# Optimization experiments

Hardware: AMD Instinct MI355X
Metric: run time of the kernel (lower is better)

## Reference

```python
import jax, jax.numpy as jnp
import numpy as np

N, E, D_IN, H = 4096, 1024, 256, 64
THETA = 0.01
LN_EPS = 1e-5


def _layer_norm(x, w, b):
    m = x.mean(-1, keepdims=True)
    v = ((x - m) ** 2).mean(-1, keepdims=True)
    return (x - m) * jax.lax.rsqrt(v + LN_EPS) * w + b


def setup_inputs() -> dict:
    key = jax.random.key(0)
    ks = jax.random.split(key, 8)
    xav = lambda k, shp: jax.random.normal(k, shp, jnp.float32) * np.float32(np.sqrt(2.0 / (shp[0] + shp[1])))
    return {
        "adj": jax.random.uniform(ks[0], (N, E), jnp.float32),
        "G": jax.random.normal(ks[1], (N, N), jnp.float32) * 0.02,
        "feats": jax.random.normal(ks[2], (N, D_IN), jnp.float32),
        "W_v_w": xav(ks[3], (H, D_IN)),
        "lin_w": xav(ks[4], (H, D_IN)),
        "w_o_w": xav(ks[5], (1, H)),
        "w_o_b": jnp.zeros((1,), jnp.float32),
        "ln1_w": jnp.ones((H,), jnp.float32),
        "ln1_b": jnp.zeros((H,), jnp.float32),
        "ln2_w": jnp.ones((H,), jnp.float32),
        "ln2_b": jnp.zeros((H,), jnp.float32),
        "kn": 10,
    }


def reference(adj, G, feats, W_v_w, lin_w, w_o_w, w_o_b, ln1_w, ln1_b, ln2_w, ln2_b, kn):
    # adj: (N, E) incidence; torch code transposes then uses adj.t() again,
    # so e_center = feats.T @ adj / edge_degree  -> (D_IN, E)
    e_center = (feats.T @ adj) / adj.sum(0)[None, :]
    f = feats @ W_v_w.T                                   # (N, H) values
    scores = (f @ f.T) / np.float32(np.sqrt(H))           # (N, N)
    attn = jax.nn.softmax(scores, axis=1)
    s = _layer_norm(e_center.T @ lin_w.T, ln1_w, ln1_b)   # (E, H)
    d = _layer_norm(attn @ f, ln2_w, ln2_b)               # (N, H)
    # hadamard_power: scores[m,n] = sum_k w[k]*(s[m,k]-d[n,k])^2 + b
    # expanded to avoid the (E*N, H) broadcast the torch code materializes
    w = w_o_w[0]                                          # (H,)
    ta = ((s * s) @ w)[:, None] + ((d * d) @ w)[None, :] - 2.0 * ((s * w) @ d.T) + w_o_b[0]
    ta = jnp.exp(-ta / np.float32(2 * 20 ** 2))           # (E, N)
    Hm = ta.T                                             # (N, E) soft incidence
    # Generate_G_from_H with unit edge weights, done via row/col scaling
    DV = Hm.sum(1)
    DE = Hm.sum(0)
    invDE = jnp.where(DE > 0, 1.0 / DE, 0.0)
    invDV = jnp.where(DV > 0, DV ** -0.5, 0.0)
    A = (invDV[:, None] * Hm) * invDE[None, :]            # DV2 @ H @ W @ invDE
    B = Hm * invDV[:, None]                               # (DV2 @ H).T side
    G_new = A @ B.T                                       # (N, N)
    return (1.0 - THETA) * G + THETA * G_new
```

## Files before the change

kernel.cpp:

```cpp
#include <hip/hip_runtime.h>
#include <hip/hip_bf16.h>
#include <math.h>

#define NN 4096
#define NE 1024
#define DIN 256
#define HD 64

typedef __hip_bfloat16 bf16;
__device__ __forceinline__ float b2f(bf16 x){ return __bfloat162float(x); }

typedef __attribute__((ext_vector_type(8))) short s16x8;
typedef __attribute__((ext_vector_type(4))) float f32x4;

__device__ __forceinline__ unsigned short f2b_rne(float x){
  unsigned u; __builtin_memcpy(&u, &x, 4);
  u += 0x7fff + ((u>>16)&1);
  return (unsigned short)(u>>16);
}

#define STAGE128(dstbase, PA, strideA, PB, strideB, k0) do{ \
  _Pragma("unroll") \
  for (int it_ = 0; it_ < 4; ++it_){ \
    int r_  = it_*32 + (t>>3); \
    int ss_ = ((t&7) ^ (r_&7))*8; \
    __builtin_amdgcn_global_load_lds( \
      (const __attribute__((address_space(1))) void*)((PA) + (size_t)r_*(strideA) + (k0) + ss_), \
      (__attribute__((address_space(3))) void*)((dstbase) + it_*4096 + t*16), 16, 0, 0); \
    __builtin_amdgcn_global_load_lds( \
      (const __attribute__((address_space(1))) void*)((PB) + (size_t)r_*(strideB) + (k0) + ss_), \
      (__attribute__((address_space(3))) void*)((dstbase) + 16384 + it_*4096 + t*16), 16, 0, 0); \
  } }while(0)

#define COMPUTE64(base) do{ \
  _Pragma("unroll") \
  for (int kk_ = 0; kk_ < 2; ++kk_){ \
    s16x8 a_[4], b_[4]; \
    _Pragma("unroll") \
    for (int mi_ = 0; mi_ < 4; ++mi_){ \
      int row_ = wr*64 + mi_*16 + (lane & 15); \
      int s_   = kk_*4 + (lane >> 4); \
      a_[mi_] = *(const s16x8*)((base) + row_*128 + ((s_ ^ (row_&7))*16)); \
    } \
    _Pragma("unroll") \
    for (int ni_ = 0; ni_ < 4; ++ni_){ \
      int row_ = wc*64 + ni_*16 + (lane & 15); \
      int s_   = kk_*4 + (lane >> 4); \
      b_[ni_] = *(const s16x8*)((base) + 16384 + row_*128 + ((s_ ^ (row_&7))*16)); \
    } \
    _Pragma("unroll") \
    for (int mi_ = 0; mi_ < 4; ++mi_) \
      _Pragma("unroll") \
      for (int ni_ = 0; ni_ < 4; ++ni_) \
        acc[mi_][ni_] = __builtin_amdgcn_mfma_f32_16x16x32_bf16(a_[mi_], b_[ni_], acc[mi_][ni_], 0, 0, 0); \
  } }while(0)

__global__ void k_t2b(const float* __restrict__ src, unsigned short* __restrict__ dst,
                      float* __restrict__ csum){
  __shared__ float Ls[64][65];
  int R = gridDim.x*64, C = gridDim.y*64;
  int r0 = blockIdx.x*64, c0 = blockIdx.y*64;
  int t = threadIdx.x;
  int lr = t>>2, lc = (t&3)*16;
  #pragma unroll
  for (int s = 0; s < 4; ++s){
    float4 v = *(const float4*)(src + (size_t)(r0+lr)*C + c0 + lc + s*4);
    Ls[lr][lc+s*4+0]=v.x; Ls[lr][lc+s*4+1]=v.y; Ls[lr][lc+s*4+2]=v.z; Ls[lr][lc+s*4+3]=v.w;
  }
  __syncthreads();
  if (csum != nullptr && t < 64){
    float s = 0.f;
    #pragma unroll
    for (int r = 0; r < 64; ++r) s += Ls[r][t];
    atomicAdd(&csum[c0 + t], s);
  }
  int wc = t>>3, wr8 = (t&7)*8;
  #pragma unroll
  for (int p = 0; p < 2; ++p){
    int c = wc + p*32;
    s16x8 o;
    #pragma unroll
    for (int e = 0; e < 8; ++e) o[e] = (short)f2b_rne(Ls[wr8+e][c]);
    *(s16x8*)(dst + (size_t)(c0+c)*R + r0 + wr8) = o;
  }
}

__global__ void __launch_bounds__(256, 2)
k_ect_mfma(const unsigned short* __restrict__ fT, const unsigned short* __restrict__ aT,
           float* __restrict__ ecT){
  __shared__ __align__(16) unsigned char sm[65536];
  const int t = threadIdx.x, lane = t & 63, w = t >> 6;
  const int wr = w >> 1, wc = w & 1;
  const int m0 = blockIdx.x*128, n0 = blockIdx.y*128, kb = blockIdx.z*256;
  const unsigned short* PA = fT + (size_t)m0*NN + kb;
  const unsigned short* PB = aT + (size_t)n0*NN + kb;
  f32x4 acc[4][4] = {};
  STAGE128(sm, PA, NN, PB, NN, 0);
  __syncthreads();
  int cur = 0;
  for (int kt = 0; kt < 4; ++kt){
    if (kt < 3) STAGE128(sm + (cur^1)*32768, PA, NN, PB, NN, (kt+1)*64);
    COMPUTE64(sm + cur*32768);
    __syncthreads();
    cur ^= 1;
  }
  #pragma unroll
  for (int mi = 0; mi < 4; ++mi)
    #pragma unroll
    for (int q = 0; q < 4; ++q){
      int c = m0 + wr*64 + mi*16 + (lane>>4)*4 + q;
      #pragma unroll
      for (int ni = 0; ni < 4; ++ni){
        int e = n0 + wc*64 + ni*16 + (lane & 15);
        atomicAdd(&ecT[(size_t)e*DIN + c], acc[mi][ni][q]);
      }
    }
}

__global__ void k_s(const float* __restrict__ ecT, const float* __restrict__ colsum,
                    const float* __restrict__ lin_w,
                    const float* __restrict__ ln1w, const float* __restrict__ ln1b,
                    const float* __restrict__ wow,
                    unsigned short* __restrict__ swb, float* __restrict__ sq_s){
  int e = blockIdx.x, h = threadIdx.x;
  const float* row = ecT + (size_t)e*DIN;
  const float* lw  = lin_w + (size_t)h*DIN;
  float acc = 0.f;
  for (int c = 0; c < DIN; ++c) acc += row[c]*lw[c];
  acc /= colsum[e];
  float tot = acc;
  for (int m=32;m>=1;m>>=1) tot += __shfl_xor(tot,m);
  float mean = tot*(1.f/64.f);
  float dv = acc - mean;
  float vv = dv*dv;
  for (int m=32;m>=1;m>>=1) vv += __shfl_xor(vv,m);
  float y = dv*(1.f/sqrtf(vv*(1.f/64.f)+1e-5f))*ln1w[h] + ln1b[h];
  float wv = wow[h];
  swb[(size_t)e*HD + h] = f2b_rne(y*wv);
  float q = wv*y*y;
  for (int m=32;m>=1;m>>=1) q += __shfl_xor(q,m);
  if (h==0) sq_s[e] = q;
}

__global__ void k_f_full(const float* __restrict__ feats, const float* __restrict__ Wv,
                         unsigned short* __restrict__ fb, unsigned short* __restrict__ fbT){
  __shared__ float As[64][65];
  __shared__ float Bs[64][65];
  __shared__ unsigned short Fs[64][72];
  int i0 = blockIdx.x*64;
  int tid=threadIdx.x, tx=tid&15, ty=tid>>4;
  float acc[4][4]={};
  for (int c0=0;c0<DIN;c0+=64){
    if (c0) __syncthreads();
    for (int idx=tid; idx<4096; idx+=256){
      int r=idx>>6, c=idx&63;
      As[c][r] = feats[(size_t)(i0+r)*DIN + c0+c];
      Bs[c][r] = Wv   [(size_t)r*DIN      + c0+c];
    }
    __syncthreads();
    for (int k=0;k<64;++k){
      float a[4], b[4];
      #pragma unroll
      for (int i=0;i<4;++i) a[i] = As[k][tx*4+i];
      #pragma unroll
      for (int i=0;i<4;++i) b[i] = Bs[k][ty*4+i];
      #pragma unroll
      for (int mi=0;mi<4;++mi)
        #pragma unroll
        for (int ni=0;ni<4;++ni) acc[mi][ni] += a[mi]*b[ni];
    }
  }
  #pragma unroll
  for (int mi=0;mi<4;++mi)
    #pragma unroll
    for (int ni=0;ni<4;++ni)
      Fs[tx*4+mi][ty*4+ni] = f2b_rne(acc[mi][ni]);
  __syncthreads();
  {
    int r = tid>>2, c0b = (tid&3)*16;
    s16x8 v0, v1;
    #pragma unroll
    for (int e=0;e<8;++e){ v0[e] = (short)Fs[r][c0b+e]; v1[e] = (short)Fs[r][c0b+8+e]; }
    *(s16x8*)(fb + (size_t)(i0+r)*HD + c0b)     = v0;
    *(s16x8*)(fb + (size_t)(i0+r)*HD + c0b + 8) = v1;
  }
  {
    int h = tid>>2, n1 = (tid&3)*16;
    s16x8 w0, w1;
    #pragma unroll
    for (int e=0;e<8;++e){ w0[e] = (short)Fs[n1+e][h]; w1[e] = (short)Fs[n1+8+e][h]; }
    *(s16x8*)(fbT + (size_t)h*NN + i0 + n1)     = w0;
    *(s16x8*)(fbT + (size_t)h*NN + i0 + n1 + 8) = w1;
  }
}

#define STAGE_ATTN(buf, j0s) do{ \
  _Pragma("unroll") \
  for (int p_=0;p_<2;++p_){ \
    int r_  = p_*32 + (t>>3); \
    int cs_ = ((t&7) ^ (r_&7))*8; \
    __builtin_amdgcn_global_load_lds( \
      (const __attribute__((address_space(1))) void*)(fb + (size_t)((j0s)+r_)*HD + cs_), \
      (__attribute__((address_space(3))) void*)(sm + (buf)*16384 + p_*4096 + t*16), 16, 0, 0); \
    __builtin_amdgcn_global_load_lds( \
      (const __attribute__((address_space(1))) void*)(fbT + (size_t)r_*NN + (j0s) + cs_), \
      (__attribute__((address_space(3))) void*)(sm + (buf)*16384 + 8192 + p_*4096 + t*16), 16, 0, 0); \
  } }while(0)

__global__ void __launch_bounds__(256)
k_attn(const unsigned short* __restrict__ fb, const unsigned short* __restrict__ fbT,
       float* __restrict__ dpre, float* __restrict__ rowsum){
  __shared__ __align__(16) unsigned char sm[49152];
  const int t  = threadIdx.x;
  const int l  = t & 63;
  const int w  = t >> 6;
  const int g  = l >> 4;
  const int i0 = blockIdx.x*64;
  const int jb0 = blockIdx.y*256;

  s16x8 aQ[2];
  {
    const unsigned short* src = fb + (size_t)(i0 + w*16 + (l&15))*HD + g*8;
    aQ[0] = *(const s16x8*)(src);
    aQ[1] = *(const s16x8*)(src + 32);
  }

  f32x4 acco[4];
  #pragma unroll
  for (int nh=0;nh<4;++nh)
    #pragma unroll
    for (int q=0;q<4;++q) acco[nh][q] = 0.f;
  float rsum[4] = {0.f,0.f,0.f,0.f};

  float* Pw = (float*)(sm + 32768 + w*4096);

  STAGE_ATTN(0, jb0);
  __syncthreads();
  int cur = 0;
  for (int jt = 0; jt < 4; ++jt){
    if (jt < 3) STAGE_ATTN(cur^1, jb0 + (jt+1)*64);
    const unsigned char* B = sm + cur*16384;

    f32x4 accs[4];
    #pragma unroll
    for (int nj=0;nj<4;++nj)
      #pragma unroll
      for (int q=0;q<4;++q) accs[nj][q] = 0.f;
    #pragma unroll
    for (int kk=0; kk<2; ++kk){
      int s = kk*4 + g;
      #pragma unroll
      for (int nj=0;nj<4;++nj){
        int row = nj*16 + (l&15);
        s16x8 b = *(const s16x8*)(B + row*128 + ((s ^ (row&7))*16));
        accs[nj] = __builtin_amdgcn_mfma_f32_16x16x32_bf16(aQ[kk], b, accs[nj], 0,0,0);
      }
    }

    #pragma unroll
    for (int q=0;q<4;++q){
      int i  = g*4 + q;
      int sw = (i&7)<<2;
      #pragma unroll
      for (int nj=0;nj<4;++nj){
        float p = __expf(accs[nj][q]*0.125f);
        rsum[q] += p;
        Pw[i*64 + ((nj*16 + (l&15)) ^ sw)] = p;
      }
    }

    #pragma unroll
    for (int kk=0; kk<2; ++kk){
      int i  = l & 15;
      int sw = (i&7)<<2;
      int jb = g*8 + kk*32;
      f32x4 va = *(const f32x4*)(Pw + i*64 + ( jb      ^ sw));
      f32x4 vb = *(const f32x4*)(Pw + i*64 + ((jb + 4) ^ sw));
      s16x8 pa;
      #pragma unroll
      for (int e=0;e<4;++e){
        float fa = va[e], fbv = vb[e];
        pa[e]   = (short)f2b_rne(fa);
        pa[4+e] = (short)f2b_rne(fbv);
      }
      int s = kk*4 + g;
      #pragma unroll
      for (int nh=0;nh<4;++nh){
        int row = nh*16 + (l&15);
        s16x8 bT = *(const s16x8*)(B + 8192 + row*128 + ((s ^ (row&7))*16));
        acco[nh] = __builtin_amdgcn_mfma_f32_16x16x32_bf16(pa, bT, acco[nh], 0,0,0);
      }
    }
    __syncthreads();
    cur ^= 1;
  }

  #pragma unroll
  for (int q=0;q<4;++q){
    float v = rsum[q];
    v += __shfl_xor(v,1); v += __shfl_xor(v,2);
    v += __shfl_xor(v,4); v += __shfl_xor(v,8);
    if ((l&15)==0) atomicAdd(&rowsum[i0 + w*16 + g*4 + q], v);
  }
  #pragma unroll
  for (int nh=0;nh<4;++nh)
    #pragma unroll
    for (int q=0;q<4;++q)
      atomicAdd(&dpre[(size_t)(i0 + w*16 + g*4 + q)*HD + nh*16 + (l&15)], acco[nh][q]);
}

__global__ void k_dln(const float* __restrict__ dpre, const float* __restrict__ rowsum,
                      const float* __restrict__ ln2w, const float* __restrict__ ln2b,
                      const float* __restrict__ wow,
                      unsigned short* __restrict__ dmatb, float* __restrict__ sq_d){
  int lane = threadIdx.x & 63;
  int n = blockIdx.x*4 + (threadIdx.x>>6);
  float x = dpre[(size_t)n*HD + lane] / rowsum[n];
  float tot = x;
  for (int m=32;m>=1;m>>=1) tot += __shfl_xor(tot,m);
  float mean = tot*(1.f/64.f);
  float dv = x - mean;
  float vv = dv*dv;
  for (int m=32;m>=1;m>>=1) vv += __shfl_xor(vv,m);
  float y = dv*(1.f/sqrtf(vv*(1.f/64.f)+1e-5f))*ln2w[lane] + ln2b[lane];
  dmatb[(size_t)n*HD + lane] = f2b_rne(y);
  float wv = wow[lane];
  float q = wv*y*y;
  for (int m=32;m>=1;m>>=1) q += __shfl_xor(q,m);
  if (lane==0) sq_d[n] = q;
}

__global__ void __launch_bounds__(256)
k_hm(const unsigned short* __restrict__ dmatb, const unsigned short* __restrict__ swb,
     const float* __restrict__ sq_d, const float* __restrict__ sq_s,
     const float* __restrict__ wob, bf16* __restrict__ Hm,
     float* __restrict__ DE, float* __restrict__ DVacc){
  __shared__ __align__(16) unsigned char sm[8192];
  __shared__ float DEp[64];
  const int t = threadIdx.x, l = t & 63, w = t >> 6, g = l >> 4;
  const int n0 = blockIdx.x*64, e0 = blockIdx.y*64;
  #pragma unroll
  for (int p = 0; p < 2; ++p){
    int r  = p*32 + (t>>3);
    int cs = ((t&7) ^ (r&7))*8;
    __builtin_amdgcn_global_load_lds(
      (const __attribute__((address_space(1))) void*)(swb + (size_t)(e0+r)*HD + cs),
      (__attribute__((address_space(3))) void*)(sm + p*4096 + t*16), 16, 0, 0);
  }
  s16x8 aQ[2];
  {
    const unsigned short* src = dmatb + (size_t)(n0 + w*16 + (l&15))*HD + g*8;
    aQ[0] = *(const s16x8*)(src);
    aQ[1] = *(const s16x8*)(src + 32);
  }
  if (t < 64) DEp[t] = 0.f;
  f32x4 accs[4];
  #pragma unroll
  for (int nj=0;nj<4;++nj)
    #pragma unroll
    for (int q=0;q<4;++q) accs[nj][q] = 0.f;
  __syncthreads();
  #pragma unroll
  for (int kk=0; kk<2; ++kk){
    int s = kk*4 + g;
    #pragma unroll
    for (int nj=0;nj<4;++nj){
      int row = nj*16 + (l&15);
      s16x8 b = *(const s16x8*)(sm + row*128 + ((s ^ (row&7))*16));
      accs[nj] = __builtin_amdgcn_mfma_f32_16x16x32_bf16(aQ[kk], b, accs[nj], 0,0,0);
    }
  }
  float bias = wob[0];
  float sqd[4];
  #pragma unroll
  for (int q=0;q<4;++q) sqd[q] = sq_d[n0 + w*16 + g*4 + q];
  float rowp[4] = {0.f,0.f,0.f,0.f};
  #pragma unroll
  for (int nj=0;nj<4;++nj){
    int e = e0 + nj*16 + (l&15);
    float sqs = sq_s[e];
    float colp = 0.f;
    #pragma unroll
    for (int q=0;q<4;++q){
      float ta = sqs + sqd[q] - 2.f*accs[nj][q] + bias;
      float arg = -ta*(1.f/800.f);
      if (!(arg > -88.f)) arg = -88.f;
      if (arg > 60.f)     arg = 60.f;
      int n = n0 + w*16 + g*4 + q;
      bf16 hv = __float2bfloat16(__expf(arg));
      Hm[(size_t)n*NE + e] = hv;
      float vr = b2f(hv);
      rowp[q] += vr;
      colp    += vr;
    }
    atomicAdd(&DEp[nj*16 + (l&15)], colp);
  }
  #pragma unroll
  for (int q=0;q<4;++q){
    float v = rowp[q];
    v += __shfl_xor(v,1); v += __shfl_xor(v,2);
    v += __shfl_xor(v,4); v += __shfl_xor(v,8);
    if ((l&15)==0) atomicAdd(&DVacc[n0 + w*16 + g*4 + q], v);
  }
  __syncthreads();
  if (t < 64) atomicAdd(&DE[e0 + t], DEp[t]);
}

__global__ void k_scale(bf16* __restrict__ Hm, const float* __restrict__ DE){
  int idx = blockIdx.x*256 + threadIdx.x;
  int row = idx >> 7, c8 = idx & 127;
  size_t base = (size_t)row*NE + c8*8;
  s16x8 v = *(const s16x8*)(Hm + base);
  s16x8 o;
  #pragma unroll
  for (int j = 0; j < 8; ++j){
    float de = DE[c8*8 + j];
    float r  = (de > 0.f) ? rsqrtf(de) : 0.f;
    unsigned int ww = ((unsigned int)(unsigned short)v[j]) << 16;
    float fv; __builtin_memcpy(&fv, &ww, 4);
    fv *= r;
    o[j] = (short)f2b_rne(fv);
  }
  *(s16x8*)(Hm + base) = o;
}

__global__ void __launch_bounds__(256, 2)
k_final(const bf16* __restrict__ A2, const float* __restrict__ DVacc,
        const float* __restrict__ G, float* __restrict__ out){
  __shared__ __align__(16) unsigned char sm[128*132*4];
  const int t    = threadIdx.x;
  const int lane = t & 63;
  const int w    = t >> 6;
  const int wr   = w >> 1, wc = w & 1;

  int bid = blockIdx.x;
  int idx = (bid & 7)*66 + (bid >> 3);
  int bi = (int)(32.5f - sqrtf(32.5f*32.5f - 2.f*(float)idx));
  while ((bi+1)*32 - ((bi+1)*bi)/2 <= idx) ++bi;
  while (bi*32 - (bi*(bi-1))/2 > idx) --bi;
  int bj = bi + (idx - (bi*32 - (bi*(bi-1))/2));
  const int i0 = bi*128, j0 = bj*128;

  const bf16* PA = A2 + (size_t)i0*NE;
  const bf16* PB = A2 + (size_t)j0*NE;

  f32x4 acc[4][4] = {};
  STAGE128(sm, PA, NE, PB, NE, 0);
  __syncthreads();
  int cur = 0;
  for (int kt = 0; kt < 16; ++kt){
    if (kt < 15) STAGE128(sm + (cur^1)*32768, PA, NE, PB, NE, (kt+1)*64);
    COMPUTE64(sm + cur*32768);
    __syncthreads();
    cur ^= 1;
  }

  float dvi[4][4], dvj[4];
  #pragma unroll
  for (int mi = 0; mi < 4; ++mi)
    #pragma unroll
    for (int q = 0; q < 4; ++q){
      float v = DVacc[i0 + wr*64 + mi*16 + (lane>>4)*4 + q];
      dvi[mi][q] = (v > 0.f) ? rsqrtf(v) : 0.f;
    }
  #pragma unroll
  for (int ni = 0; ni < 4; ++ni){
    float v = DVacc[j0 + wc*64 + ni*16 + (lane & 15)];
    dvj[ni] = (v > 0.f) ? rsqrtf(v) : 0.f;
  }

  float (*T)[132] = (float(*)[132])sm;
  #pragma unroll
  for (int mi = 0; mi < 4; ++mi)
    #pragma unroll
    for (int ni = 0; ni < 4; ++ni)
      #pragma unroll
      for (int q = 0; q < 4; ++q)
        T[wr*64 + mi*16 + (lane>>4)*4 + q][wc*64 + ni*16 + (lane & 15)] =
          0.01f*(dvi[mi][q]*dvj[ni]*acc[mi][ni][q]);
  __syncthreads();

  #pragma unroll
  for (int it = 0; it < 16; ++it){
    int idx2 = it*256 + t;
    int il = idx2 >> 5;
    int jc = (idx2 & 31)*4;
    size_t o = (size_t)(i0+il)*NN + j0 + jc;
    float4 gv = *(const float4*)(G + o);
    float4 r;
    r.x = 0.99f*gv.x + T[il][jc+0];
    r.y = 0.99f*gv.y + T[il][jc+1];
    r.z = 0.99f*gv.z + T[il][jc+2];
    r.w = 0.99f*gv.w + T[il][jc+3];
    *(float4*)(out + o) = r;
  }

  if (bi == bj) return;
  __syncthreads();
  #pragma unroll
  for (int mi = 0; mi < 4; ++mi)
    #pragma unroll
    for (int ni = 0; ni < 4; ++ni)
      #pragma unroll
      for (int q = 0; q < 4; ++q)
        T[wc*64 + ni*16 + (lane & 15)][wr*64 + mi*16 + (lane>>4)*4 + q] =
          0.01f*(dvi[mi][q]*dvj[ni]*acc[mi][ni][q]);
  __syncthreads();
  #pragma unroll
  for (int it = 0; it < 16; ++it){
    int idx2 = it*256 + t;
    int jl = idx2 >> 5;
    int ic = (idx2 & 31)*4;
    size_t o = (size_t)(j0+jl)*NN + i0 + ic;
    float4 gv = *(const float4*)(G + o);
    float4 r;
    r.x = 0.99f*gv.x + T[jl][ic+0];
    r.y = 0.99f*gv.y + T[jl][ic+1];
    r.z = 0.99f*gv.z + T[jl][ic+2];
    r.w = 0.99f*gv.w + T[jl][ic+3];
    *(float4*)(out + o) = r;
  }
}

extern "C" void kernel_launch(void* const* d_in, const int* in_sizes, int n_in,
                              void* d_out, int out_size, void* d_ws, size_t ws_size,
                              hipStream_t stream){
  const float* adj  = (const float*)d_in[0];
  const float* G    = (const float*)d_in[1];
  const float* feats= (const float*)d_in[2];
  const float* Wv   = (const float*)d_in[3];
  const float* lin  = (const float*)d_in[4];
  const float* wow  = (const float*)d_in[5];
  const float* wob  = (const float*)d_in[6];
  const float* ln1w = (const float*)d_in[7];
  const float* ln1b = (const float*)d_in[8];
  const float* ln2w = (const float*)d_in[9];
  const float* ln2b = (const float*)d_in[10];
  float* out = (float*)d_out;

  float* w = (float*)d_ws;
  float* colsum = w; w += NE;
  float* DE     = w; w += NE;
  float* sq_s   = w; w += NE;
  float* rowsum = w; w += NN;
  float* sq_d   = w; w += NN;
  float* DVacc  = w; w += NN;
  float* ecT    = w; w += NE*DIN;
  float* dpre   = w; w += NN*HD;
  unsigned short* swb    = (unsigned short*)w; w += NE*HD/2;
  unsigned short* dmatb  = (unsigned short*)w; w += NN*HD/2;
  unsigned short* fbm    = (unsigned short*)w; w += NN*HD/2;
  unsigned short* fbT    = (unsigned short*)w; w += NN*HD/2;
  unsigned short* featsT = (unsigned short*)w; w += NN*DIN/2;
  bf16*  Hm     = (bf16*)w;
  unsigned short* adjT = (unsigned short*)Hm;

  hipMemsetAsync(colsum, 0, NE*sizeof(float), stream);
  hipMemsetAsync(DE,     0, NE*sizeof(float), stream);
  hipMemsetAsync(rowsum, 0, NN*sizeof(float), stream);
  hipMemsetAsync(DVacc,  0, NN*sizeof(float), stream);
  hipMemsetAsync(ecT,    0, (size_t)NE*DIN*sizeof(float), stream);
  hipMemsetAsync(dpre,   0, (size_t)NN*HD*sizeof(float), stream);

  k_t2b     <<<dim3(64,4),   256, 0, stream>>>(feats, featsT, nullptr);
  k_t2b     <<<dim3(64,16),  256, 0, stream>>>(adj, adjT, colsum);
  k_ect_mfma<<<dim3(2,8,16), 256, 0, stream>>>(featsT, adjT, ecT);
  k_s       <<<NE,            64, 0, stream>>>(ecT, colsum, lin, ln1w, ln1b, wow, swb, sq_s);
  k_f_full  <<<64,           256, 0, stream>>>(feats, Wv, fbm, fbT);
  k_attn    <<<dim3(64,16),  256, 0, stream>>>(fbm, fbT, dpre, rowsum);
  k_dln     <<<NN/4,         256, 0, stream>>>(dpre, rowsum, ln2w, ln2b, wow, dmatb, sq_d);
  k_hm      <<<dim3(64,16),  256, 0, stream>>>(dmatb, swb, sq_d, sq_s, wob, Hm, DE, DVacc);
  k_scale   <<<2048,         256, 0, stream>>>(Hm, DE);
  k_final   <<<528,          256, 0, stream>>>(Hm, DVacc, G, out);
}
```

Measured before the change: 339.7 us.

## Merge prep kernels, split atomic accumulators into partial buffers, fuse LN kernels

```diff
diff --git a/kernel.cpp b/kernel.cpp
--- a/kernel.cpp
+++ b/kernel.cpp
@@ -55,45 +55,104 @@
         acc[mi_][ni_] = __builtin_amdgcn_mfma_f32_16x16x32_bf16(a_[mi_], b_[ni_], acc[mi_][ni_], 0, 0, 0); \
   } }while(0)
 
-__global__ void k_t2b(const float* __restrict__ src, unsigned short* __restrict__ dst,
-                      float* __restrict__ csum){
-  __shared__ float Ls[64][65];
-  int R = gridDim.x*64, C = gridDim.y*64;
-  int r0 = blockIdx.x*64, c0 = blockIdx.y*64;
-  int t = threadIdx.x;
-  int lr = t>>2, lc = (t&3)*16;
-  #pragma unroll
-  for (int s = 0; s < 4; ++s){
-    float4 v = *(const float4*)(src + (size_t)(r0+lr)*C + c0 + lc + s*4);
-    Ls[lr][lc+s*4+0]=v.x; Ls[lr][lc+s*4+1]=v.y; Ls[lr][lc+s*4+2]=v.z; Ls[lr][lc+s*4+3]=v.w;
-  }
-  __syncthreads();
-  if (csum != nullptr && t < 64){
-    float s = 0.f;
-    #pragma unroll
-    for (int r = 0; r < 64; ++r) s += Ls[r][t];
-    atomicAdd(&csum[c0 + t], s);
-  }
-  int wc = t>>3, wr8 = (t&7)*8;
-  #pragma unroll
-  for (int p = 0; p < 2; ++p){
-    int c = wc + p*32;
-    s16x8 o;
-    #pragma unroll
-    for (int e = 0; e < 8; ++e) o[e] = (short)f2b_rne(Ls[wr8+e][c]);
-    *(s16x8*)(dst + (size_t)(c0+c)*R + r0 + wr8) = o;
+__global__ void __launch_bounds__(256)
+k_prep(const float* __restrict__ feats, const float* __restrict__ adj,
+       const float* __restrict__ Wv,
+       unsigned short* __restrict__ featsT, unsigned short* __restrict__ adjT,
+       float* __restrict__ colsum,
+       unsigned short* __restrict__ fb, unsigned short* __restrict__ fbT){
+  __shared__ __align__(16) unsigned char smp[42496];
+  const int b = blockIdx.x, t = threadIdx.x;
+  if (b < 1280){
+    const float* src; unsigned short* dst; float* csum; int R, C, bx, by;
+    if (b < 256){ src=feats; dst=featsT; csum=nullptr; R=NN; C=DIN; bx=b&63;  by=b>>6; }
+    else { int bb=b-256; src=adj; dst=adjT; csum=colsum; R=NN; C=NE; bx=bb&63; by=bb>>6; }
+    float (*Ls)[65] = (float(*)[65])smp;
+    int r0 = bx*64, c0 = by*64;
+    int lr = t>>2, lc = (t&3)*16;
+    #pragma unroll
+    for (int s = 0; s < 4; ++s){
+      float4 v = *(const float4*)(src + (size_t)(r0+lr)*C + c0 + lc + s*4);
+      Ls[lr][lc+s*4+0]=v.x; Ls[lr][lc+s*4+1]=v.y; Ls[lr][lc+s*4+2]=v.z; Ls[lr][lc+s*4+3]=v.w;
+    }
+    __syncthreads();
+    if (csum != nullptr && t < 64){
+      float s = 0.f;
+      #pragma unroll
+      for (int r = 0; r < 64; ++r) s += Ls[r][t];
+      atomicAdd(&csum[c0 + t], s);
+    }
+    int wcx = t>>3, wr8 = (t&7)*8;
+    #pragma unroll
+    for (int p = 0; p < 2; ++p){
+      int c = wcx + p*32;
+      s16x8 o;
+      #pragma unroll
+      for (int e = 0; e < 8; ++e) o[e] = (short)f2b_rne(Ls[wr8+e][c]);
+      *(s16x8*)(dst + (size_t)(c0+c)*R + r0 + wr8) = o;
+    }
+  } else {
+    float (*As)[65] = (float(*)[65])smp;
+    float (*Bs)[65] = (float(*)[65])(smp + 16640);
+    unsigned short (*Fs)[72] = (unsigned short(*)[72])(smp + 33280);
+    int i0 = (b-1280)*64;
+    int tx = t&15, ty = t>>4;
+    float acc[4][4] = {};
+    for (int c0 = 0; c0 < DIN; c0 += 64){
+      if (c0) __syncthreads();
+      for (int idx = t; idx < 4096; idx += 256){
+        int r = idx>>6, c = idx&63;
+        As[c][r] = feats[(size_t)(i0+r)*DIN + c0+c];
+        Bs[c][r] = Wv   [(size_t)r*DIN      + c0+c];
+      }
+      __syncthreads();
+      for (int k = 0; k < 64; ++k){
+        float a[4], bb[4];
+        #pragma unroll
+        for (int i=0;i<4;++i) a[i]  = As[k][tx*4+i];
+        #pragma unroll
+        for (int i=0;i<4;++i) bb[i] = Bs[k][ty*4+i];
+        #pragma unroll
+        for (int mi=0;mi<4;++mi)
+          #pragma unroll
+          for (int ni=0;ni<4;++ni) acc[mi][ni] += a[mi]*bb[ni];
+      }
+    }
+    #pragma unroll
+    for (int mi=0;mi<4;++mi)
+      #pragma unroll
+      for (int ni=0;ni<4;++ni)
+        Fs[tx*4+mi][ty*4+ni] = f2b_rne(acc[mi][ni]);
+    __syncthreads();
+    {
+      int r = t>>2, c0b = (t&3)*16;
+      s16x8 v0, v1;
+      #pragma unroll
+      for (int e=0;e<8;++e){ v0[e] = (short)Fs[r][c0b+e]; v1[e] = (short)Fs[r][c0b+8+e]; }
+      *(s16x8*)(fb + (size_t)(i0+r)*HD + c0b)     = v0;
+      *(s16x8*)(fb + (size_t)(i0+r)*HD + c0b + 8) = v1;
+    }
+    {
+      int h = t>>2, n1 = (t&3)*16;
+      s16x8 w0, w1;
+      #pragma unroll
+      for (int e=0;e<8;++e){ w0[e] = (short)Fs[n1+e][h]; w1[e] = (short)Fs[n1+8+e][h]; }
+      *(s16x8*)(fbT + (size_t)h*NN + i0 + n1)     = w0;
+      *(s16x8*)(fbT + (size_t)h*NN + i0 + n1 + 8) = w1;
+    }
   }
 }
 
 __global__ void __launch_bounds__(256, 2)
 k_ect_mfma(const unsigned short* __restrict__ fT, const unsigned short* __restrict__ aT,
-           float* __restrict__ ecT){
+           float* __restrict__ ecT4){
   __shared__ __align__(16) unsigned char sm[65536];
   const int t = threadIdx.x, lane = t & 63, w = t >> 6;
   const int wr = w >> 1, wc = w & 1;
   const int m0 = blockIdx.x*128, n0 = blockIdx.y*128, kb = blockIdx.z*256;
   const unsigned short* PA = fT + (size_t)m0*NN + kb;
   const unsigned short* PB = aT + (size_t)n0*NN + kb;
+  float* ep = ecT4 + (size_t)(blockIdx.z>>2)*NE*DIN;
   f32x4 acc[4][4] = {};
   STAGE128(sm, PA, NN, PB, NN, 0);
   __syncthreads();
@@ -112,86 +171,9 @@
       #pragma unroll
       for (int ni = 0; ni < 4; ++ni){
         int e = n0 + wc*64 + ni*16 + (lane & 15);
-        atomicAdd(&ecT[(size_t)e*DIN + c], acc[mi][ni][q]);
-      }
-    }
-}
-
-__global__ void k_s(const float* __restrict__ ecT, const float* __restrict__ colsum,
-                    const float* __restrict__ lin_w,
-                    const float* __restrict__ ln1w, const float* __restrict__ ln1b,
-                    const float* __restrict__ wow,
-                    unsigned short* __restrict__ swb, float* __restrict__ sq_s){
-  int e = blockIdx.x, h = threadIdx.x;
-  const float* row = ecT + (size_t)e*DIN;
-  const float* lw  = lin_w + (size_t)h*DIN;
-  float acc = 0.f;
-  for (int c = 0; c < DIN; ++c) acc += row[c]*lw[c];
-  acc /= colsum[e];
-  float tot = acc;
-  for (int m=32;m>=1;m>>=1) tot += __shfl_xor(tot,m);
-  float mean = tot*(1.f/64.f);
-  float dv = acc - mean;
-  float vv = dv*dv;
-  for (int m=32;m>=1;m>>=1) vv += __shfl_xor(vv,m);
-  float y = dv*(1.f/sqrtf(vv*(1.f/64.f)+1e-5f))*ln1w[h] + ln1b[h];
-  float wv = wow[h];
-  swb[(size_t)e*HD + h] = f2b_rne(y*wv);
-  float q = wv*y*y;
-  for (int m=32;m>=1;m>>=1) q += __shfl_xor(q,m);
-  if (h==0) sq_s[e] = q;
-}
-
-__global__ void k_f_full(const float* __restrict__ feats, const float* __restrict__ Wv,
-                         unsigned short* __restrict__ fb, unsigned short* __restrict__ fbT){
-  __shared__ float As[64][65];
-  __shared__ float Bs[64][65];
-  __shared__ unsigned short Fs[64][72];
-  int i0 = blockIdx.x*64;
-  int tid=threadIdx.x, tx=tid&15, ty=tid>>4;
-  float acc[4][4]={};
-  for (int c0=0;c0<DIN;c0+=64){
-    if (c0) __syncthreads();
-    for (int idx=tid; idx<4096; idx+=256){
-      int r=idx>>6, c=idx&63;
-      As[c][r] = feats[(size_t)(i0+r)*DIN + c0+c];
-      Bs[c][r] = Wv   [(size_t)r*DIN      + c0+c];
-    }
-    __syncthreads();
-    for (int k=0;k<64;++k){
-      float a[4], b[4];
-      #pragma unroll
-      for (int i=0;i<4;++i) a[i] = As[k][tx*4+i];
-      #pragma unroll
-      for (int i=0;i<4;++i) b[i] = Bs[k][ty*4+i];
-      #pragma unroll
-      for (int mi=0;mi<4;++mi)
-        #pragma unroll
-        for (int ni=0;ni<4;++ni) acc[mi][ni] += a[mi]*b[ni];
-    }
-  }
-  #pragma unroll
-  for (int mi=0;mi<4;++mi)
-    #pragma unroll
-    for (int ni=0;ni<4;++ni)
-      Fs[tx*4+mi][ty*4+ni] = f2b_rne(acc[mi][ni]);
-  __syncthreads();
-  {
-    int r = tid>>2, c0b = (tid&3)*16;
-    s16x8 v0, v1;
-    #pragma unroll
-    for (int e=0;e<8;++e){ v0[e] = (short)Fs[r][c0b+e]; v1[e] = (short)Fs[r][c0b+8+e]; }
-    *(s16x8*)(fb + (size_t)(i0+r)*HD + c0b)     = v0;
-    *(s16x8*)(fb + (size_t)(i0+r)*HD + c0b + 8) = v1;
-  }
-  {
-    int h = tid>>2, n1 = (tid&3)*16;
-    s16x8 w0, w1;
-    #pragma unroll
-    for (int e=0;e<8;++e){ w0[e] = (short)Fs[n1+e][h]; w1[e] = (short)Fs[n1+8+e][h]; }
-    *(s16x8*)(fbT + (size_t)h*NN + i0 + n1)     = w0;
-    *(s16x8*)(fbT + (size_t)h*NN + i0 + n1 + 8) = w1;
-  }
+        atomicAdd(&ep[(size_t)e*DIN + c], acc[mi][ni][q]);
+      }
+    }
 }
 
 #define STAGE_ATTN(buf, j0s) do{ \
@@ -209,7 +191,7 @@
 
 __global__ void __launch_bounds__(256)
 k_attn(const unsigned short* __restrict__ fb, const unsigned short* __restrict__ fbT,
-       float* __restrict__ dpre, float* __restrict__ rowsum){
+       float* __restrict__ dpre_p, float* __restrict__ rowsum){
   __shared__ __align__(16) unsigned char sm[49152];
   const int t  = threadIdx.x;
   const int l  = t & 63;
@@ -217,6 +199,7 @@
   const int g  = l >> 4;
   const int i0 = blockIdx.x*64;
   const int jb0 = blockIdx.y*256;
+  float* dp = dpre_p + (size_t)(blockIdx.y & 7)*NN*HD;
 
   s16x8 aQ[2];
   {
@@ -306,28 +289,66 @@
   for (int nh=0;nh<4;++nh)
     #pragma unroll
     for (int q=0;q<4;++q)
-      atomicAdd(&dpre[(size_t)(i0 + w*16 + g*4 + q)*HD + nh*16 + (l&15)], acco[nh][q]);
-}
-
-__global__ void k_dln(const float* __restrict__ dpre, const float* __restrict__ rowsum,
-                      const float* __restrict__ ln2w, const float* __restrict__ ln2b,
-                      const float* __restrict__ wow,
-                      unsigned short* __restrict__ dmatb, float* __restrict__ sq_d){
-  int lane = threadIdx.x & 63;
-  int n = blockIdx.x*4 + (threadIdx.x>>6);
-  float x = dpre[(size_t)n*HD + lane] / rowsum[n];
-  float tot = x;
-  for (int m=32;m>=1;m>>=1) tot += __shfl_xor(tot,m);
-  float mean = tot*(1.f/64.f);
-  float dv = x - mean;
-  float vv = dv*dv;
-  for (int m=32;m>=1;m>>=1) vv += __shfl_xor(vv,m);
-  float y = dv*(1.f/sqrtf(vv*(1.f/64.f)+1e-5f))*ln2w[lane] + ln2b[lane];
-  dmatb[(size_t)n*HD + lane] = f2b_rne(y);
-  float wv = wow[lane];
-  float q = wv*y*y;
-  for (int m=32;m>=1;m>>=1) q += __shfl_xor(q,m);
-  if (lane==0) sq_d[n] = q;
+      atomicAdd(&dp[(size_t)(i0 + w*16 + g*4 + q)*HD + nh*16 + (l&15)], acco[nh][q]);
+}
+
+__global__ void __launch_bounds__(256)
+k_sd(const float* __restrict__ ecT4, const float* __restrict__ colsum,
+     const float* __restrict__ lin_w,
+     const float* __restrict__ ln1w, const float* __restrict__ ln1b,
+     const float* __restrict__ wow,
+     unsigned short* __restrict__ swb, float* __restrict__ sq_s,
+     const float* __restrict__ dpre_p, const float* __restrict__ rowsum,
+     const float* __restrict__ ln2w, const float* __restrict__ ln2b,
+     unsigned short* __restrict__ dmatb, float* __restrict__ sq_d){
+  __shared__ float Lw[64][257];
+  const int b = blockIdx.x, t = threadIdx.x;
+  if (b < 256){
+    for (int idx = t; idx < 64*DIN; idx += 256) Lw[idx>>8][idx&255] = lin_w[idx];
+    __syncthreads();
+    int w = t>>6, h = t&63;
+    int e = b*4 + w;
+    const float* r0 = ecT4 + (size_t)e*DIN;
+    float acc = 0.f;
+    #pragma unroll 4
+    for (int c = 0; c < DIN; ++c){
+      float rv = r0[c] + r0[(size_t)NE*DIN + c]
+               + r0[2*(size_t)NE*DIN + c] + r0[3*(size_t)NE*DIN + c];
+      acc += rv * Lw[h][c];
+    }
+    acc /= colsum[e];
+    float tot = acc;
+    for (int m=32;m>=1;m>>=1) tot += __shfl_xor(tot,m);
+    float mean = tot*(1.f/64.f);
+    float dv = acc - mean;
+    float vv = dv*dv;
+    for (int m=32;m>=1;m>>=1) vv += __shfl_xor(vv,m);
+    float y = dv*(1.f/sqrtf(vv*(1.f/64.f)+1e-5f))*ln1w[h] + ln1b[h];
+    float wv = wow[h];
+    swb[(size_t)e*HD + h] = f2b_rne(y*wv);
+    float q = wv*y*y;
+    for (int m=32;m>=1;m>>=1) q += __shfl_xor(q,m);
+    if (h==0) sq_s[e] = q;
+  } else {
+    int lane = t & 63;
+    int n = (b-256)*4 + (t>>6);
+    float x = 0.f;
+    #pragma unroll
+    for (int p = 0; p < 8; ++p) x += dpre_p[(size_t)p*NN*HD + (size_t)n*HD + lane];
+    x /= rowsum[n];
+    float tot = x;
+    for (int m=32;m>=1;m>>=1) tot += __shfl_xor(tot,m);
+    float mean = tot*(1.f/64.f);
+    float dv = x - mean;
+    float vv = dv*dv;
+    for (int m=32;m>=1;m>>=1) vv += __shfl_xor(vv,m);
+    float y = dv*(1.f/sqrtf(vv*(1.f/64.f)+1e-5f))*ln2w[lane] + ln2b[lane];
+    dmatb[(size_t)n*HD + lane] = f2b_rne(y);
+    float wv = wow[lane];
+    float q = wv*y*y;
+    for (int m=32;m>=1;m>>=1) q += __shfl_xor(q,m);
+    if (lane==0) sq_d[n] = q;
+  }
 }
 
 __global__ void __launch_bounds__(256)
@@ -545,8 +566,7 @@
   float* rowsum = w; w += NN;
   float* sq_d   = w; w += NN;
   float* DVacc  = w; w += NN;
-  float* ecT    = w; w += NE*DIN;
-  float* dpre   = w; w += NN*HD;
+  float* ecT4   = w; w += 4*(size_t)NE*DIN;
   unsigned short* swb    = (unsigned short*)w; w += NE*HD/2;
   unsigned short* dmatb  = (unsigned short*)w; w += NN*HD/2;
   unsigned short* fbm    = (unsigned short*)w; w += NN*HD/2;
@@ -554,21 +574,20 @@
   unsigned short* featsT = (unsigned short*)w; w += NN*DIN/2;
   bf16*  Hm     = (bf16*)w;
   unsigned short* adjT = (unsigned short*)Hm;
+  float* dpre_p = (float*)Hm;
 
   hipMemsetAsync(colsum, 0, NE*sizeof(float), stream);
   hipMemsetAsync(DE,     0, NE*sizeof(float), stream);
   hipMemsetAsync(rowsum, 0, NN*sizeof(float), stream);
   hipMemsetAsync(DVacc,  0, NN*sizeof(float), stream);
-  hipMemsetAsync(ecT,    0, (size_t)NE*DIN*sizeof(float), stream);
-  hipMemsetAsync(dpre,   0, (size_t)NN*HD*sizeof(float), stream);
-
-  k_t2b     <<<dim3(64,4),   256, 0, stream>>>(feats, featsT, nullptr);
-  k_t2b     <<<dim3(64,16),  256, 0, stream>>>(adj, adjT, colsum);
-  k_ect_mfma<<<dim3(2,8,16), 256, 0, stream>>>(featsT, adjT, ecT);
-  k_s       <<<NE,            64, 0, stream>>>(ecT, colsum, lin, ln1w, ln1b, wow, swb, sq_s);
-  k_f_full  <<<64,           256, 0, stream>>>(feats, Wv, fbm, fbT);
-  k_attn    <<<dim3(64,16),  256, 0, stream>>>(fbm, fbT, dpre, rowsum);
-  k_dln     <<<NN/4,         256, 0, stream>>>(dpre, rowsum, ln2w, ln2b, wow, dmatb, sq_d);
+  hipMemsetAsync(ecT4,   0, 4*(size_t)NE*DIN*sizeof(float), stream);
+
+  k_prep    <<<1344,         256, 0, stream>>>(feats, adj, Wv, featsT, adjT, colsum, fbm, fbT);
+  k_ect_mfma<<<dim3(2,8,16), 256, 0, stream>>>(featsT, adjT, ecT4);
+  hipMemsetAsync(dpre_p, 0, 8*(size_t)NN*HD*sizeof(float), stream);
+  k_attn    <<<dim3(64,16),  256, 0, stream>>>(fbm, fbT, dpre_p, rowsum);
+  k_sd      <<<1280,         256, 0, stream>>>(ecT4, colsum, lin, ln1w, ln1b, wow, swb, sq_s,
+                                               dpre_p, rowsum, ln2w, ln2b, dmatb, sq_d);
   k_hm      <<<dim3(64,16),  256, 0, stream>>>(dmatb, swb, sq_d, sq_s, wob, Hm, DE, DVacc);
   k_scale   <<<2048,         256, 0, stream>>>(Hm, DE);
   k_final   <<<528,          256, 0, stream>>>(Hm, DVacc, G, out);
```

New measurement: 338.8 us. No clear change (-0.3%).
